# Kernel tuning notes

Hardware: AMD Instinct MI355X
Metric: run time of the kernel (lower is better)

## Reference

```python
import jax, jax.numpy as jnp
import numpy as np

N_LEVELS = 9

def _avg_pool_2x2(x):
    # tf.nn.avg_pool2d(ksize=2, strides=2, padding='SAME'); H,W even at every
    # level for H=W=512, so SAME == VALID == simple 2x2 mean.
    b, h, w, c = x.shape
    return x.reshape(b, h // 2, 2, w // 2, 2, c).mean(axis=(2, 4))

def setup_inputs() -> dict:
    key = jax.random.key(0)
    x = jax.random.normal(key, (8, 512, 512, 2), dtype=jnp.float32)
    return {"x": x}

def reference(x):
    B, H, W, C = x.shape
    levels = [x]
    cur = x
    for _ in range(N_LEVELS - 1):
        cur = _avg_pool_2x2(cur)
        levels.append(cur)
    # tf.image.resize bilinear (half-pixel centers, no antialias on upsample)
    # == jax.image.resize method='bilinear' for upscaling.
    ups = [jax.image.resize(lv, (B, H, W, C), method='bilinear') for lv in levels]
    stacked = jnp.concatenate(ups, axis=-1)          # [B, H, W, 9*C]
    stacked = stacked[:, None]                       # [B, 1, H, W, 9*C]
    return jnp.transpose(stacked, (0, 4, 2, 3, 1))   # [B, 9*C, H, W, 1]
```

## Files before the change

kernel.cpp:

```cpp
#include <hip/hip_runtime.h>


#define HWTOT (512 * 512)
#define RW 260

typedef float vfloat4 __attribute__((ext_vector_type(4)));

__constant__ int c_off2[7] = {0, 0, 524288, 655360, 688128, 696320, 698368};

__global__ __launch_bounds__(256) void build_lv01(const float* __restrict__ x,
                                                  float2* __restrict__ pyr,
                                                  float* __restrict__ out) {
  const int b = blockIdx.y;
  const int tx = blockIdx.x & 7;
  const int ty = blockIdx.x >> 3;
  const int t = threadIdx.x;
  const int i = t >> 4;
  const int j = t & 15;
  const int xr = ty * 32 + 2 * i;
  const int xc = tx * 64 + 4 * j;
  const float* r0 = x + ((size_t)(b * 512 + xr) * 512 + xc) * 2;
  const float* r1 = r0 + 1024;
  float4 a0 = *(const float4*)r0;
  float4 a1 = *(const float4*)(r0 + 4);
  float4 c0 = *(const float4*)r1;
  float4 c1 = *(const float4*)(r1 + 4);
  float2 o0 = {(a0.x + a0.z + c0.x + c0.z) * 0.25f, (a0.y + a0.w + c0.y + c0.w) * 0.25f};
  float2 o1 = {(a1.x + a1.z + c1.x + c1.z) * 0.25f, (a1.y + a1.w + c1.y + c1.w) * 0.25f};
  float2* g = pyr + ((size_t)(b * 256 + ty * 16 + i) * 256 + tx * 32 + 2 * j);
  *(vfloat4*)g = (vfloat4){o0.x, o0.y, o1.x, o1.y};
  const size_t ob = (size_t)(b * 18) * HWTOT + (size_t)xr * 512 + xc;
  *(vfloat4*)(out + ob) = (vfloat4){a0.x, a0.z, a1.x, a1.z};
  *(vfloat4*)(out + ob + 512) = (vfloat4){c0.x, c0.z, c1.x, c1.z};
  *(vfloat4*)(out + ob + HWTOT) = (vfloat4){a0.y, a0.w, a1.y, a1.w};
  *(vfloat4*)(out + ob + HWTOT + 512) = (vfloat4){c0.y, c0.w, c1.y, c1.w};
}

__global__ __launch_bounds__(256) void build_lv2_6(float2* pyr) {
  const int b = blockIdx.y;
  const int tx = blockIdx.x & 7, ty = blockIdx.x >> 3;
  const int t = threadIdx.x;

  __shared__ float2 sh1[32 * 32];
  __shared__ float2 sh2[16 * 16];
  __shared__ float2 sh3[8 * 8];
  __shared__ float2 sh4[4 * 4];
  __shared__ float2 sh5[2 * 2];

  {
    const int row = t >> 3, c4 = (t & 7) << 2;
    const float2* src = pyr + (size_t)(b * 256 + ty * 32 + row) * 256 + tx * 32 + c4;
    float4 v0 = *(const float4*)src;
    float4 v1 = *(const float4*)(src + 2);
    *(float4*)&sh1[t * 4] = v0;
    *(float4*)&sh1[t * 4 + 2] = v1;
  }
  __syncthreads();
  {
    const int i = t >> 4, j = t & 15;
    float2 a = sh1[(2 * i) * 32 + 2 * j], c = sh1[(2 * i) * 32 + 2 * j + 1];
    float2 d = sh1[(2 * i + 1) * 32 + 2 * j], e = sh1[(2 * i + 1) * 32 + 2 * j + 1];
    float2 o = {(a.x + c.x + d.x + e.x) * 0.25f, (a.y + c.y + d.y + e.y) * 0.25f};
    sh2[i * 16 + j] = o;
    pyr[524288 + (size_t)(b * 128 + ty * 16 + i) * 128 + tx * 16 + j] = o;
  }
  __syncthreads();
  if (t < 64) {
    const int i = t >> 3, j = t & 7;
    float2 a = sh2[(2 * i) * 16 + 2 * j], c = sh2[(2 * i) * 16 + 2 * j + 1];
    float2 d = sh2[(2 * i + 1) * 16 + 2 * j], e = sh2[(2 * i + 1) * 16 + 2 * j + 1];
    float2 o = {(a.x + c.x + d.x + e.x) * 0.25f, (a.y + c.y + d.y + e.y) * 0.25f};
    sh3[i * 8 + j] = o;
    pyr[655360 + (size_t)(b * 64 + ty * 8 + i) * 64 + tx * 8 + j] = o;
  }
  __syncthreads();
  if (t < 16) {
    const int i = t >> 2, j = t & 3;
    float2 a = sh3[(2 * i) * 8 + 2 * j], c = sh3[(2 * i) * 8 + 2 * j + 1];
    float2 d = sh3[(2 * i + 1) * 8 + 2 * j], e = sh3[(2 * i + 1) * 8 + 2 * j + 1];
    float2 o = {(a.x + c.x + d.x + e.x) * 0.25f, (a.y + c.y + d.y + e.y) * 0.25f};
    sh4[i * 4 + j] = o;
    pyr[688128 + (size_t)(b * 32 + ty * 4 + i) * 32 + tx * 4 + j] = o;
  }
  __syncthreads();
  if (t < 4) {
    const int i = t >> 1, j = t & 1;
    float2 a = sh4[(2 * i) * 4 + 2 * j], c = sh4[(2 * i) * 4 + 2 * j + 1];
    float2 d = sh4[(2 * i + 1) * 4 + 2 * j], e = sh4[(2 * i + 1) * 4 + 2 * j + 1];
    float2 o = {(a.x + c.x + d.x + e.x) * 0.25f, (a.y + c.y + d.y + e.y) * 0.25f};
    sh5[i * 2 + j] = o;
    pyr[696320 + (size_t)(b * 16 + ty * 2 + i) * 16 + tx * 2 + j] = o;
  }
  __syncthreads();
  if (t == 0) {
    float2 a = sh5[0], c = sh5[1], d = sh5[2], e = sh5[3];
    float2 o = {(a.x + c.x + d.x + e.x) * 0.25f, (a.y + c.y + d.y + e.y) * 0.25f};
    pyr[698368 + (size_t)(b * 8 + ty) * 8 + tx] = o;
  }
}

__global__ __launch_bounds__(256) void upsample_lv(const float2* __restrict__ pyr,
                                                   float* __restrict__ out) {
  const int t = threadIdx.x;
  const int tp = t & 127;
  const int rr0 = t >> 7;
  const int w0pix = tp << 2;
  const int bx = blockIdx.x;
  const int b = blockIdx.y;
  const int lv = blockIdx.z + 1;
  const int S = 512 >> lv;
  const float scale = 1.0f / (float)(1 << lv);

  __shared__ float2 rows[4 * RW + 20];

  const int W = S + 2;
  const int hbase = (int)floorf(((float)(bx << 2) + 0.5f) * scale - 0.5f);

  if (lv <= 6) {
#pragma unroll
    for (int r = 0; r < 4; ++r) {
      int sr = hbase + r;
      sr = sr < 0 ? 0 : (sr > S - 1 ? S - 1 : sr);
      const float2* src = pyr + c_off2[lv] + (size_t)b * S * S + (size_t)sr * S;
      for (int c = t; c < W; c += 256) {
        int sc = c - 1;
        sc = sc < 0 ? 0 : (sc > S - 1 ? S - 1 : sc);
        rows[r * RW + c] = src[sc];
      }
    }
  } else {
    float2* img7 = rows + 4 * RW;
    float2* img8 = img7 + 16;
    const float2* l6 = pyr + 698368 + (size_t)b * 64;
    if (t < 16) {
      const int i = t >> 2, j = t & 3;
      float2 a = l6[(2 * i) * 8 + 2 * j], c = l6[(2 * i) * 8 + 2 * j + 1];
      float2 d = l6[(2 * i + 1) * 8 + 2 * j], e = l6[(2 * i + 1) * 8 + 2 * j + 1];
      img7[t] = {(a.x + c.x + d.x + e.x) * 0.25f, (a.y + c.y + d.y + e.y) * 0.25f};
    }
    __syncthreads();
    if (lv == 8 && t < 4) {
      const int i = t >> 1, j = t & 1;
      float2 a = img7[(2 * i) * 4 + 2 * j], c = img7[(2 * i) * 4 + 2 * j + 1];
      float2 d = img7[(2 * i + 1) * 4 + 2 * j], e = img7[(2 * i + 1) * 4 + 2 * j + 1];
      img8[t] = {(a.x + c.x + d.x + e.x) * 0.25f, (a.y + c.y + d.y + e.y) * 0.25f};
    }
    __syncthreads();
    const float2* img = (lv == 7) ? img7 : img8;
    if (t < 4 * W) {
      int r, c;
      if (lv == 7) {
        r = t / 6;
        c = t - r * 6;
      } else {
        r = t >> 2;
        c = t & 3;
      }
      int sr = hbase + r;
      sr = sr < 0 ? 0 : (sr > S - 1 ? S - 1 : sr);
      int sc = c - 1;
      sc = sc < 0 ? 0 : (sc > S - 1 ? S - 1 : sc);
      rows[r * RW + c] = img[sr * S + sc];
    }
  }
  __syncthreads();

  const size_t obase0 =
      (size_t)(b * 18 + 2 * lv) * HWTOT + (size_t)((bx << 2) + rr0) * 512 + w0pix;

  if (lv == 1) {
    const int e0 = tp << 1;
#pragma unroll
    for (int dr2 = 0; dr2 < 2; ++dr2) {
      const int rr = rr0 + 2 * dr2;
      const int d0 = (rr + 1) >> 1;
      const float fh = (rr & 1) ? 0.25f : 0.75f;
      const float wy0 = 1.0f - fh;
      const float2* R0 = rows + d0 * RW + e0;
      const float2* R1 = R0 + RW;
      float2 p0 = R0[0], p1 = R0[1], p2 = R0[2], p3 = R0[3];
      float2 q0 = R1[0], q1 = R1[1], q2 = R1[2], q3 = R1[3];
      float hx0 = p0.x * 0.25f + p1.x * 0.75f, hy0 = p0.y * 0.25f + p1.y * 0.75f;
      float hx1 = p1.x * 0.75f + p2.x * 0.25f, hy1 = p1.y * 0.75f + p2.y * 0.25f;
      float hx2 = p1.x * 0.25f + p2.x * 0.75f, hy2 = p1.y * 0.25f + p2.y * 0.75f;
      float hx3 = p2.x * 0.75f + p3.x * 0.25f, hy3 = p2.y * 0.75f + p3.y * 0.25f;
      float gx0 = q0.x * 0.25f + q1.x * 0.75f, gy0 = q0.y * 0.25f + q1.y * 0.75f;
      float gx1 = q1.x * 0.75f + q2.x * 0.25f, gy1 = q1.y * 0.75f + q2.y * 0.25f;
      float gx2 = q1.x * 0.25f + q2.x * 0.75f, gy2 = q1.y * 0.25f + q2.y * 0.75f;
      float gx3 = q2.x * 0.75f + q3.x * 0.25f, gy3 = q2.y * 0.75f + q3.y * 0.25f;
      const size_t ob = obase0 + (size_t)dr2 * 1024;
      *(vfloat4*)(out + ob) = (vfloat4){hx0 * wy0 + gx0 * fh, hx1 * wy0 + gx1 * fh,
                                        hx2 * wy0 + gx2 * fh, hx3 * wy0 + gx3 * fh};
      *(vfloat4*)(out + ob + HWTOT) = (vfloat4){hy0 * wy0 + gy0 * fh, hy1 * wy0 + gy1 * fh,
                                                hy2 * wy0 + gy2 * fh, hy3 * wy0 + gy3 * fh};
    }
    return;
  }

  int w0l[4];
  float fw[4];
#pragma unroll
  for (int k = 0; k < 4; ++k) {
    float sw = ((float)(w0pix + k) + 0.5f) * scale - 0.5f;
    float f = floorf(sw);
    fw[k] = sw - f;
    w0l[k] = (int)f + 1;
  }
#pragma unroll
  for (int dr2 = 0; dr2 < 2; ++dr2) {
    const int rr = rr0 + 2 * dr2;
    const int h = (bx << 2) + rr;
    float shf = ((float)h + 0.5f) * scale - 0.5f;
    float f0 = floorf(shf);
    float fh = shf - f0;
    int d0 = (int)f0 - hbase;
    const float2* R0 = rows + d0 * RW;
    const float2* R1 = R0 + RW;
    const float wy0 = 1.0f - fh;
    float o0[4], o1[4];
#pragma unroll
    for (int k = 0; k < 4; ++k) {
      float2 v00 = R0[w0l[k]], v01 = R0[w0l[k] + 1];
      float2 v10 = R1[w0l[k]], v11 = R1[w0l[k] + 1];
      float wx0 = 1.0f - fw[k];
      float tx_ = v00.x * wx0 + v01.x * fw[k];
      float bx_ = v10.x * wx0 + v11.x * fw[k];
      float ty_ = v00.y * wx0 + v01.y * fw[k];
      float by_ = v10.y * wx0 + v11.y * fw[k];
      o0[k] = tx_ * wy0 + bx_ * fh;
      o1[k] = ty_ * wy0 + by_ * fh;
    }
    const size_t ob = obase0 + (size_t)dr2 * 1024;
    *(vfloat4*)(out + ob) = (vfloat4){o0[0], o0[1], o0[2], o0[3]};
    *(vfloat4*)(out + ob + HWTOT) = (vfloat4){o1[0], o1[1], o1[2], o1[3]};
  }
}

extern "C" void kernel_launch(void* const* d_in, const int* in_sizes, int n_in,
                              void* d_out, int out_size, void* d_ws, size_t ws_size,
                              hipStream_t stream) {
  const float* x = (const float*)d_in[0];
  float* out = (float*)d_out;
  float2* pyr = (float2*)d_ws;

  build_lv01<<<dim3(128, 8), 256, 0, stream>>>(x, pyr, out);
  build_lv2_6<<<dim3(64, 8), 256, 0, stream>>>(pyr);
  upsample_lv<<<dim3(128, 8, 8), 256, 0, stream>>>(pyr, out);
}
```

Before: 166.8 us.

## Fuse pyramid build kernels and double output rows per upsample block

Merges the level-0/1 pooling kernel into the level 2-6 pyramid kernel, so level 1 is computed from x straight into shared memory instead of being written to and re-read from global memory. This also drops one launch. The upsample kernel now produces 8 output rows per block instead of 4, with 6 cached source rows, halving its grid. Level-1 rows get a padded shared-memory index to reduce bank conflicts. The cost is fewer blocks in both kernels, so occupancy and parallelism are lower, and more work falls on each thread.

```diff
diff --git a/kernel.cpp b/kernel.cpp
--- a/kernel.cpp
+++ b/kernel.cpp
@@ -2,41 +2,15 @@
 
 
 #define HWTOT (512 * 512)
-#define RW 260
+#define RW 292
 
 typedef float vfloat4 __attribute__((ext_vector_type(4)));
 
 __constant__ int c_off2[7] = {0, 0, 524288, 655360, 688128, 696320, 698368};
 
-__global__ __launch_bounds__(256) void build_lv01(const float* __restrict__ x,
-                                                  float2* __restrict__ pyr,
-                                                  float* __restrict__ out) {
-  const int b = blockIdx.y;
-  const int tx = blockIdx.x & 7;
-  const int ty = blockIdx.x >> 3;
-  const int t = threadIdx.x;
-  const int i = t >> 4;
-  const int j = t & 15;
-  const int xr = ty * 32 + 2 * i;
-  const int xc = tx * 64 + 4 * j;
-  const float* r0 = x + ((size_t)(b * 512 + xr) * 512 + xc) * 2;
-  const float* r1 = r0 + 1024;
-  float4 a0 = *(const float4*)r0;
-  float4 a1 = *(const float4*)(r0 + 4);
-  float4 c0 = *(const float4*)r1;
-  float4 c1 = *(const float4*)(r1 + 4);
-  float2 o0 = {(a0.x + a0.z + c0.x + c0.z) * 0.25f, (a0.y + a0.w + c0.y + c0.w) * 0.25f};
-  float2 o1 = {(a1.x + a1.z + c1.x + c1.z) * 0.25f, (a1.y + a1.w + c1.y + c1.w) * 0.25f};
-  float2* g = pyr + ((size_t)(b * 256 + ty * 16 + i) * 256 + tx * 32 + 2 * j);
-  *(vfloat4*)g = (vfloat4){o0.x, o0.y, o1.x, o1.y};
-  const size_t ob = (size_t)(b * 18) * HWTOT + (size_t)xr * 512 + xc;
-  *(vfloat4*)(out + ob) = (vfloat4){a0.x, a0.z, a1.x, a1.z};
-  *(vfloat4*)(out + ob + 512) = (vfloat4){c0.x, c0.z, c1.x, c1.z};
-  *(vfloat4*)(out + ob + HWTOT) = (vfloat4){a0.y, a0.w, a1.y, a1.w};
-  *(vfloat4*)(out + ob + HWTOT + 512) = (vfloat4){c0.y, c0.w, c1.y, c1.w};
-}
-
-__global__ __launch_bounds__(256) void build_lv2_6(float2* pyr) {
+__global__ __launch_bounds__(256) void build_levels_1_6(const float* __restrict__ x,
+                                                        float2* __restrict__ pyr,
+                                                        float* __restrict__ out) {
   const int b = blockIdx.y;
   const int tx = blockIdx.x & 7, ty = blockIdx.x >> 3;
   const int t = threadIdx.x;
@@ -48,12 +22,35 @@
   __shared__ float2 sh5[2 * 2];
 
   {
-    const int row = t >> 3, c4 = (t & 7) << 2;
-    const float2* src = pyr + (size_t)(b * 256 + ty * 32 + row) * 256 + tx * 32 + c4;
-    float4 v0 = *(const float4*)src;
-    float4 v1 = *(const float4*)(src + 2);
-    *(float4*)&sh1[t * 4] = v0;
-    *(float4*)&sh1[t * 4 + 2] = v1;
+    const int i = t >> 3;
+    const int j0 = (t & 7) << 2;
+    const int row0 = ty * 64 + 2 * i;
+    const int colx = tx * 64 + 2 * j0;
+    const float* r0 = x + (((size_t)(b * 512 + row0)) * 512 + colx) * 2;
+    const float* r1 = r0 + 1024;
+    float4 a[4], c[4];
+    float2 o[4];
+#pragma unroll
+    for (int k = 0; k < 4; ++k) {
+      a[k] = *(const float4*)(r0 + 4 * k);
+      c[k] = *(const float4*)(r1 + 4 * k);
+      o[k].x = (a[k].x + a[k].z + c[k].x + c[k].z) * 0.25f;
+      o[k].y = (a[k].y + a[k].w + c[k].y + c[k].w) * 0.25f;
+      sh1[i * 32 + j0 + k] = o[k];
+    }
+    float2* g = pyr + ((size_t)(b * 256 + ty * 32 + i) * 256 + tx * 32 + j0);
+    *(float4*)(g) = make_float4(o[0].x, o[0].y, o[1].x, o[1].y);
+    *(float4*)(g + 2) = make_float4(o[2].x, o[2].y, o[3].x, o[3].y);
+
+    const size_t ob = (size_t)(b * 18) * HWTOT + (size_t)row0 * 512 + colx;
+    *(vfloat4*)(out + ob)                  = (vfloat4){a[0].x, a[0].z, a[1].x, a[1].z};
+    *(vfloat4*)(out + ob + 4)              = (vfloat4){a[2].x, a[2].z, a[3].x, a[3].z};
+    *(vfloat4*)(out + ob + 512)            = (vfloat4){c[0].x, c[0].z, c[1].x, c[1].z};
+    *(vfloat4*)(out + ob + 512 + 4)        = (vfloat4){c[2].x, c[2].z, c[3].x, c[3].z};
+    *(vfloat4*)(out + ob + HWTOT)          = (vfloat4){a[0].y, a[0].w, a[1].y, a[1].w};
+    *(vfloat4*)(out + ob + HWTOT + 4)      = (vfloat4){a[2].y, a[2].w, a[3].y, a[3].w};
+    *(vfloat4*)(out + ob + HWTOT + 512)    = (vfloat4){c[0].y, c[0].w, c[1].y, c[1].w};
+    *(vfloat4*)(out + ob + HWTOT + 512 + 4)= (vfloat4){c[2].y, c[2].w, c[3].y, c[3].w};
   }
   __syncthreads();
   {
@@ -111,25 +108,37 @@
   const int S = 512 >> lv;
   const float scale = 1.0f / (float)(1 << lv);
 
-  __shared__ float2 rows[4 * RW + 20];
+  __shared__ float2 rows[6 * RW + 20];
 
   const int W = S + 2;
-  const int hbase = (int)floorf(((float)(bx << 2) + 0.5f) * scale - 0.5f);
-
-  if (lv <= 6) {
-#pragma unroll
-    for (int r = 0; r < 4; ++r) {
+  const int hbase = (int)floorf(((float)(bx << 3) + 0.5f) * scale - 0.5f);
+
+  if (lv == 1) {
+#pragma unroll
+    for (int r = 0; r < 6; ++r) {
+      int sr = hbase + r;
+      sr = sr < 0 ? 0 : (sr > S - 1 ? S - 1 : sr);
+      const float2* src = pyr + (size_t)b * S * S + (size_t)sr * S;
+      for (int c = t; c < W; c += 256) {
+        int sc = c - 1;
+        sc = sc < 0 ? 0 : (sc > S - 1 ? S - 1 : sc);
+        rows[r * RW + c + (c >> 3)] = src[sc];
+      }
+    }
+  } else if (lv <= 6) {
+#pragma unroll
+    for (int r = 0; r < 6; ++r) {
       int sr = hbase + r;
       sr = sr < 0 ? 0 : (sr > S - 1 ? S - 1 : sr);
       const float2* src = pyr + c_off2[lv] + (size_t)b * S * S + (size_t)sr * S;
-      for (int c = t; c < W; c += 256) {
-        int sc = c - 1;
+      if (t < W) {
+        int sc = t - 1;
         sc = sc < 0 ? 0 : (sc > S - 1 ? S - 1 : sc);
-        rows[r * RW + c] = src[sc];
+        rows[r * RW + t] = src[sc];
       }
     }
   } else {
-    float2* img7 = rows + 4 * RW;
+    float2* img7 = rows + 6 * RW;
     float2* img8 = img7 + 16;
     const float2* l6 = pyr + 698368 + (size_t)b * 64;
     if (t < 16) {
@@ -147,15 +156,9 @@
     }
     __syncthreads();
     const float2* img = (lv == 7) ? img7 : img8;
-    if (t < 4 * W) {
-      int r, c;
-      if (lv == 7) {
-        r = t / 6;
-        c = t - r * 6;
-      } else {
-        r = t >> 2;
-        c = t & 3;
-      }
+    if (t < 6 * W) {
+      int r = t / W;
+      int c = t - r * W;
       int sr = hbase + r;
       sr = sr < 0 ? 0 : (sr > S - 1 ? S - 1 : sr);
       int sc = c - 1;
@@ -166,20 +169,24 @@
   __syncthreads();
 
   const size_t obase0 =
-      (size_t)(b * 18 + 2 * lv) * HWTOT + (size_t)((bx << 2) + rr0) * 512 + w0pix;
+      (size_t)(b * 18 + 2 * lv) * HWTOT + (size_t)((bx << 3) + rr0) * 512 + w0pix;
 
   if (lv == 1) {
     const int e0 = tp << 1;
-#pragma unroll
-    for (int dr2 = 0; dr2 < 2; ++dr2) {
+    const int i0 = e0 + (e0 >> 3);
+    const int i1 = (e0 + 1) + ((e0 + 1) >> 3);
+    const int i2 = (e0 + 2) + ((e0 + 2) >> 3);
+    const int i3 = (e0 + 3) + ((e0 + 3) >> 3);
+#pragma unroll
+    for (int dr2 = 0; dr2 < 4; ++dr2) {
       const int rr = rr0 + 2 * dr2;
       const int d0 = (rr + 1) >> 1;
       const float fh = (rr & 1) ? 0.25f : 0.75f;
       const float wy0 = 1.0f - fh;
-      const float2* R0 = rows + d0 * RW + e0;
+      const float2* R0 = rows + d0 * RW;
       const float2* R1 = R0 + RW;
-      float2 p0 = R0[0], p1 = R0[1], p2 = R0[2], p3 = R0[3];
-      float2 q0 = R1[0], q1 = R1[1], q2 = R1[2], q3 = R1[3];
+      float2 p0 = R0[i0], p1 = R0[i1], p2 = R0[i2], p3 = R0[i3];
+      float2 q0 = R1[i0], q1 = R1[i1], q2 = R1[i2], q3 = R1[i3];
       float hx0 = p0.x * 0.25f + p1.x * 0.75f, hy0 = p0.y * 0.25f + p1.y * 0.75f;
       float hx1 = p1.x * 0.75f + p2.x * 0.25f, hy1 = p1.y * 0.75f + p2.y * 0.25f;
       float hx2 = p1.x * 0.25f + p2.x * 0.75f, hy2 = p1.y * 0.25f + p2.y * 0.75f;
@@ -207,9 +214,9 @@
     w0l[k] = (int)f + 1;
   }
 #pragma unroll
-  for (int dr2 = 0; dr2 < 2; ++dr2) {
+  for (int dr2 = 0; dr2 < 4; ++dr2) {
     const int rr = rr0 + 2 * dr2;
-    const int h = (bx << 2) + rr;
+    const int h = (bx << 3) + rr;
     float shf = ((float)h + 0.5f) * scale - 0.5f;
     float f0 = floorf(shf);
     float fh = shf - f0;
@@ -243,7 +250,6 @@
   float* out = (float*)d_out;
   float2* pyr = (float2*)d_ws;
 
-  build_lv01<<<dim3(128, 8), 256, 0, stream>>>(x, pyr, out);
-  build_lv2_6<<<dim3(64, 8), 256, 0, stream>>>(pyr);
-  upsample_lv<<<dim3(128, 8, 8), 256, 0, stream>>>(pyr, out);
+  build_levels_1_6<<<dim3(64, 8), 256, 0, stream>>>(x, pyr, out);
+  upsample_lv<<<dim3(64, 8, 8), 256, 0, stream>>>(pyr, out);
 }
```

After: 164.7 us. About the same (-1.2%).
